# Optimization experiments

Measured on AMD Instinct MI355X. Metric: run time of the kernel, lower is better.

Reference implementation:

```python
import jax, jax.numpy as jnp
import numpy as np
import math

B_CH = 128   # bottleneck channels (conv1x1 in)
N_CH = 256   # encoder filters (conv1x1 out / linear in)
L = 16       # filter length (linear out); hop = L//2
BATCH = 8
K = 32000    # number of frames
T_ORIGIN = (L // 2) * (K - 1) + L  # 256008


def setup_inputs() -> dict:
    key = jax.random.key(0)
    k1, k2, k3, k4 = jax.random.split(key, 4)
    return {
        "mixture_w": jax.random.normal(k1, (BATCH, N_CH, K), jnp.float32),
        "est_mask": jax.random.normal(k2, (BATCH, B_CH, K), jnp.float32),
        "W_mask": jax.random.normal(k3, (N_CH, B_CH), jnp.float32) * (1.0 / np.sqrt(B_CH)),
        "W_basis": jax.random.normal(k4, (L, N_CH), jnp.float32) * (1.0 / np.sqrt(N_CH)),
        "T_origin": T_ORIGIN,
    }


def overlap_and_add(signal, frame_step):
    # signal: [..., frames, frame_length]
    frames, frame_length = signal.shape[-2], signal.shape[-1]
    sub_len = math.gcd(frame_length, frame_step)
    sub_step = frame_step // sub_len
    spf = frame_length // sub_len  # subframes per frame
    out_size = frame_step * (frames - 1) + frame_length
    out_sub = out_size // sub_len
    sub_sig = signal.reshape(signal.shape[:-2] + (frames * spf, sub_len))
    # scatter index for each subframe (same as torch unfold + index_add_)
    idx = (jnp.arange(frames)[:, None] * sub_step + jnp.arange(spf)[None, :]).reshape(-1)
    res = jnp.zeros(signal.shape[:-2] + (out_sub, sub_len), signal.dtype)
    res = res.at[..., idx, :].add(sub_sig)
    return res.reshape(signal.shape[:-2] + (out_size,))


def reference(mixture_w, est_mask, W_mask, W_basis, T_origin):
    # conv1x1 (bias-free) == channel matmul: [B_CH -> N_CH]
    m = jnp.einsum('nb,gbk->gnk', W_mask, est_mask)   # [batch, N, K]
    x = mixture_w * jax.nn.relu(m)                    # masked encoder output
    # transpose + Linear(N -> L, no bias): [batch, K, L]
    x = jnp.einsum('gnk,ln->gkl', x, W_basis)
    est_source = overlap_and_add(x, L // 2)           # [batch, T_conv]
    pad = T_origin - est_source.shape[-1]
    return jnp.pad(est_source, ((0, 0), (0, pad)))
```

## Files before the change

### kernel.cpp

```cpp
#include <hip/hip_runtime.h>
#include <stdint.h>

#define BATCH 8
#define NCH 256
#define BCH 128
#define KFR 32000
#define TOUT 256008
#define KT 32
#define NTPB 8
#define CHUNK (KT * NTPB)
#define NCHUNK (KFR / CHUNK)

typedef __attribute__((ext_vector_type(8))) short bf16x8;
typedef __attribute__((ext_vector_type(4))) float f32x4;

__device__ __forceinline__ unsigned short f32_to_bf16(float f) {
    unsigned int u = __builtin_bit_cast(unsigned int, f);
    u += 0x7FFFu + ((u >> 16) & 1u);
    return (unsigned short)(u >> 16);
}
__device__ __forceinline__ unsigned int pack2(float a, float b) {
    return (unsigned int)f32_to_bf16(a) | ((unsigned int)f32_to_bf16(b) << 16);
}
__device__ __forceinline__ f32x4 mload(const float* p) {
    f32x4 v;
    v[0] = p[0];
    v[1] = p[(size_t)KFR];
    v[2] = p[(size_t)2 * KFR];
    v[3] = p[(size_t)3 * KFR];
    return v;
}

__global__ void convert_weights(const float* __restrict__ Wm,
                                const float* __restrict__ Wb,
                                unsigned short* __restrict__ wbf) {
    int i = blockIdx.x * 256 + threadIdx.x;
    if (i < NCH * BCH) wbf[i] = f32_to_bf16(Wm[i]);
    if (i < 16 * NCH)  wbf[NCH * BCH + i] = f32_to_bf16(Wb[i]);
}

#define ESTT_W 68
#define XT_W 132
#define ESTT_WORDS (KT * ESTT_W)
#define XT_WORDS (KT * XT_W)
#define LOC_FLOATS (8 * CHUNK + 8)

#define G1(NT, FT, MM) { \
    const unsigned short* wr = wbf + (64 * wv + 16 * (NT) + l15) * BCH + 8 * lq; \
    bf16x8 w0 = *reinterpret_cast<const bf16x8*>(wr); \
    bf16x8 w1 = *reinterpret_cast<const bf16x8*>(wr + 32); \
    bf16x8 w2 = *reinterpret_cast<const bf16x8*>(wr + 64); \
    bf16x8 w3 = *reinterpret_cast<const bf16x8*>(wr + 96); \
    int f = 16 * (FT) + l15; \
    int msk = (2 * (FT) + (l15 >> 3)) & 3; \
    const unsigned short* br = estT + f * (2 * ESTT_W); \
    f32x4 a = {0.f, 0.f, 0.f, 0.f}; \
    a = __builtin_amdgcn_mfma_f32_16x16x32_bf16(w0, *reinterpret_cast<const bf16x8*>(br + 8 * ((0  + lq) ^ msk)), a, 0, 0, 0); \
    a = __builtin_amdgcn_mfma_f32_16x16x32_bf16(w1, *reinterpret_cast<const bf16x8*>(br + 8 * ((4  + lq) ^ msk)), a, 0, 0, 0); \
    a = __builtin_amdgcn_mfma_f32_16x16x32_bf16(w2, *reinterpret_cast<const bf16x8*>(br + 8 * ((8  + lq) ^ msk)), a, 0, 0, 0); \
    a = __builtin_amdgcn_mfma_f32_16x16x32_bf16(w3, *reinterpret_cast<const bf16x8*>(br + 8 * ((12 + lq) ^ msk)), a, 0, 0, 0); \
    float x0 = (a[0] > 0.f) ? (MM)[0] * a[0] : 0.f; \
    float x1 = (a[1] > 0.f) ? (MM)[1] * a[1] : 0.f; \
    float x2 = (a[2] > 0.f) ? (MM)[2] * a[2] : 0.f; \
    float x3 = (a[3] > 0.f) ? (MM)[3] * a[3] : 0.f; \
    int v = 8 * wv + 2 * (NT) + (lq >> 1); \
    uint2 uu; uu.x = pack2(x0, x1); uu.y = pack2(x2, x3); \
    *reinterpret_cast<uint2*>(xtd + f * XT_W + ((v ^ msk) << 2) + 2 * (lq & 1)) = uu; \
}

__global__ __launch_bounds__(256, 4)
void fused_decoder(const float* __restrict__ mix,
                   const float* __restrict__ est,
                   const unsigned short* __restrict__ wbf,
                   float* __restrict__ out) {
    __shared__ __align__(16) unsigned int smem[ESTT_WORDS + XT_WORDS + LOC_FLOATS];
    unsigned int* estd = smem;
    unsigned int* xtd  = smem + ESTT_WORDS;
    unsigned short* estT = reinterpret_cast<unsigned short*>(estd);
    unsigned short* xt   = reinterpret_cast<unsigned short*>(xtd);
    float* locout = reinterpret_cast<float*>(smem + ESTT_WORDS + XT_WORDS);

    const int tid = threadIdx.x;
    const int lane = tid & 63;
    const int wv = tid >> 6;
    const int l15 = lane & 15;
    const int lq = lane >> 4;
    const int f4 = tid & 7;
    const int rbase = tid >> 3;

    const int bid = blockIdx.x;
    const int g = bid / NCHUNK;
    const int c = bid % NCHUNK;

    const float* eg0 = est + ((size_t)g * BCH) * KFR + c * CHUNK;
    const float* mg0 = mix + ((size_t)g * NCH) * KFR + c * CHUNK;

    for (int s = tid; s < LOC_FLOATS / 4; s += 256) {
        f32x4 z = {0.f, 0.f, 0.f, 0.f};
        *reinterpret_cast<f32x4*>(locout + 4 * s) = z;
    }

    f32x4 er00, er01, er10, er11;
    {
        int bp0 = rbase, bp1 = 32 + rbase;
        er00 = *reinterpret_cast<const f32x4*>(eg0 + (size_t)(2 * bp0) * KFR + 4 * f4);
        er01 = *reinterpret_cast<const f32x4*>(eg0 + (size_t)(2 * bp0 + 1) * KFR + 4 * f4);
        er10 = *reinterpret_cast<const f32x4*>(eg0 + (size_t)(2 * bp1) * KFR + 4 * f4);
        er11 = *reinterpret_cast<const f32x4*>(eg0 + (size_t)(2 * bp1 + 1) * KFR + 4 * f4);
    }

    for (int t = 0; t < NTPB; ++t) {
        const float* mg = mg0 + t * KT;

        {
            int msk = (f4 >> 1) & 3;
            int base0 = (((rbase >> 2) ^ msk) << 2) + (rbase & 3);
            int base1 = ((((32 + rbase) >> 2) ^ msk) << 2) + ((32 + rbase) & 3);
#pragma unroll
            for (int i = 0; i < 4; ++i) {
                estd[(4 * f4 + i) * ESTT_W + base0] = pack2(er00[i], er01[i]);
                estd[(4 * f4 + i) * ESTT_W + base1] = pack2(er10[i], er11[i]);
            }
        }
        __syncthreads();

        const float* pm = mg + (size_t)(64 * wv + 4 * lq) * KFR + l15;
        f32x4 ma0 = mload(pm);
        f32x4 ma1 = mload(pm + (size_t)16 * KFR);
        f32x4 ma2 = mload(pm + (size_t)32 * KFR);
        f32x4 ma3 = mload(pm + (size_t)48 * KFR);
        G1(0, 0, ma0)
        G1(1, 0, ma1)
        f32x4 mb0 = mload(pm + 16);
        f32x4 mb1 = mload(pm + (size_t)16 * KFR + 16);
        f32x4 mb2 = mload(pm + (size_t)32 * KFR + 16);
        f32x4 mb3 = mload(pm + (size_t)48 * KFR + 16);
        G1(2, 0, ma2)
        G1(3, 0, ma3)
        G1(0, 1, mb0)
        G1(1, 1, mb1)
        G1(2, 1, mb2)
        G1(3, 1, mb3)
        __syncthreads();

        {
            const float* egn = eg0 + (t + 1 < NTPB ? (t + 1) * KT : t * KT);
            int bp0 = rbase, bp1 = 32 + rbase;
            er00 = *reinterpret_cast<const f32x4*>(egn + (size_t)(2 * bp0) * KFR + 4 * f4);
            er01 = *reinterpret_cast<const f32x4*>(egn + (size_t)(2 * bp0 + 1) * KFR + 4 * f4);
            er10 = *reinterpret_cast<const f32x4*>(egn + (size_t)(2 * bp1) * KFR + 4 * f4);
            er11 = *reinterpret_cast<const f32x4*>(egn + (size_t)(2 * bp1 + 1) * KFR + 4 * f4);
        }
        f32x4 acc2 = {0.f, 0.f, 0.f, 0.f};
        if (wv < 2) {
            int f = 16 * wv + l15;
            int msk = (2 * wv + (l15 >> 3)) & 3;
#pragma unroll
            for (int ks = 0; ks < 8; ++ks) {
                bf16x8 a = *reinterpret_cast<const bf16x8*>(
                    wbf + NCH * BCH + l15 * NCH + 32 * ks + 8 * lq);
                bf16x8 b = *reinterpret_cast<const bf16x8*>(
                    xt + f * (2 * XT_W) + 8 * ((4 * ks + lq) ^ msk));
                acc2 = __builtin_amdgcn_mfma_f32_16x16x32_bf16(a, b, acc2, 0, 0, 0);
            }
        }
        if (wv < 2 && lq < 2) {
            int f = 16 * wv + l15;
            int base = 256 * t + 8 * f + 4 * lq;
#pragma unroll
            for (int r = 0; r < 4; ++r) locout[base + r] += acc2[r];
        }
        __syncthreads();
        if (wv < 2 && lq >= 2) {
            int f = 16 * wv + l15;
            int base = 256 * t + 8 * f + 4 * lq;
#pragma unroll
            for (int r = 0; r < 4; ++r) locout[base + r] += acc2[r];
        }
    }
    __syncthreads();

    {
        float* og = out + (size_t)g * TOUT + (size_t)(8 * CHUNK) * c;
        for (int s = tid; s < LOC_FLOATS / 4; s += 256) {
            f32x4 v = *reinterpret_cast<const f32x4*>(locout + 4 * s);
            if (s >= 2 && s < (LOC_FLOATS / 4 - 2)) {
                *reinterpret_cast<f32x4*>(og + 4 * s) = v;
            } else {
#pragma unroll
                for (int r = 0; r < 4; ++r) atomicAdd(og + 4 * s + r, v[r]);
            }
        }
    }
}

extern "C" void kernel_launch(void* const* d_in, const int* in_sizes, int n_in,
                              void* d_out, int out_size, void* d_ws, size_t ws_size,
                              hipStream_t stream) {
    const float* mix = (const float*)d_in[0];
    const float* est = (const float*)d_in[1];
    const float* Wm  = (const float*)d_in[2];
    const float* Wb  = (const float*)d_in[3];
    unsigned short* wbf = (unsigned short*)d_ws;

    hipMemsetAsync(d_out, 0, (size_t)out_size * sizeof(float), stream);
    convert_weights<<<128, 256, 0, stream>>>(Wm, Wb, wbf);
    fused_decoder<<<BATCH * NCHUNK, 256, 0, stream>>>(mix, est, wbf, (float*)d_out);
}
```

Before: 140.5 us.

## Shrink per-block tile, drop LDS padding with XOR swizzle, shuffle-combine overlap-add

Result: slower. 304.4 us (+116.6%).

```diff
diff --git a/kernel.cpp b/kernel.cpp
--- a/kernel.cpp
+++ b/kernel.cpp
@@ -7,9 +7,12 @@
 #define KFR 32000
 #define TOUT 256008
 #define KT 32
-#define NTPB 8
+#define NTPB 5
 #define CHUNK (KT * NTPB)
 #define NCHUNK (KFR / CHUNK)
+#define ESTW 64
+#define XTW 128
+#define LOC_FLOATS (8 * CHUNK + 8)
 
 typedef __attribute__((ext_vector_type(8))) short bf16x8;
 typedef __attribute__((ext_vector_type(4))) float f32x4;
@@ -30,6 +33,9 @@
     v[3] = p[(size_t)3 * KFR];
     return v;
 }
+__device__ __forceinline__ int swz(int row, int w) {
+    return (((w >> 2) ^ (((row >> 2) & 3) << 1)) << 2) | (w & 3);
+}
 
 __global__ void convert_weights(const float* __restrict__ Wm,
                                 const float* __restrict__ Wb,
@@ -38,12 +44,6 @@
     if (i < NCH * BCH) wbf[i] = f32_to_bf16(Wm[i]);
     if (i < 16 * NCH)  wbf[NCH * BCH + i] = f32_to_bf16(Wb[i]);
 }
-
-#define ESTT_W 68
-#define XT_W 132
-#define ESTT_WORDS (KT * ESTT_W)
-#define XT_WORDS (KT * XT_W)
-#define LOC_FLOATS (8 * CHUNK + 8)
 
 #define G1(NT, FT, MM) { \
     const unsigned short* wr = wbf + (64 * wv + 16 * (NT) + l15) * BCH + 8 * lq; \
@@ -52,33 +52,31 @@
     bf16x8 w2 = *reinterpret_cast<const bf16x8*>(wr + 64); \
     bf16x8 w3 = *reinterpret_cast<const bf16x8*>(wr + 96); \
     int f = 16 * (FT) + l15; \
-    int msk = (2 * (FT) + (l15 >> 3)) & 3; \
-    const unsigned short* br = estT + f * (2 * ESTT_W); \
+    int sg = ((f >> 2) & 3) << 1; \
+    const unsigned int* br = estd + f * ESTW; \
     f32x4 a = {0.f, 0.f, 0.f, 0.f}; \
-    a = __builtin_amdgcn_mfma_f32_16x16x32_bf16(w0, *reinterpret_cast<const bf16x8*>(br + 8 * ((0  + lq) ^ msk)), a, 0, 0, 0); \
-    a = __builtin_amdgcn_mfma_f32_16x16x32_bf16(w1, *reinterpret_cast<const bf16x8*>(br + 8 * ((4  + lq) ^ msk)), a, 0, 0, 0); \
-    a = __builtin_amdgcn_mfma_f32_16x16x32_bf16(w2, *reinterpret_cast<const bf16x8*>(br + 8 * ((8  + lq) ^ msk)), a, 0, 0, 0); \
-    a = __builtin_amdgcn_mfma_f32_16x16x32_bf16(w3, *reinterpret_cast<const bf16x8*>(br + 8 * ((12 + lq) ^ msk)), a, 0, 0, 0); \
+    a = __builtin_amdgcn_mfma_f32_16x16x32_bf16(w0, *reinterpret_cast<const bf16x8*>(br + (((0  + lq) ^ sg) << 2)), a, 0, 0, 0); \
+    a = __builtin_amdgcn_mfma_f32_16x16x32_bf16(w1, *reinterpret_cast<const bf16x8*>(br + (((4  + lq) ^ sg) << 2)), a, 0, 0, 0); \
+    a = __builtin_amdgcn_mfma_f32_16x16x32_bf16(w2, *reinterpret_cast<const bf16x8*>(br + (((8  + lq) ^ sg) << 2)), a, 0, 0, 0); \
+    a = __builtin_amdgcn_mfma_f32_16x16x32_bf16(w3, *reinterpret_cast<const bf16x8*>(br + (((12 + lq) ^ sg) << 2)), a, 0, 0, 0); \
     float x0 = (a[0] > 0.f) ? (MM)[0] * a[0] : 0.f; \
     float x1 = (a[1] > 0.f) ? (MM)[1] * a[1] : 0.f; \
     float x2 = (a[2] > 0.f) ? (MM)[2] * a[2] : 0.f; \
     float x3 = (a[3] > 0.f) ? (MM)[3] * a[3] : 0.f; \
-    int v = 8 * wv + 2 * (NT) + (lq >> 1); \
+    int ue = 8 * wv + 2 * (NT) + (lq >> 1); \
     uint2 uu; uu.x = pack2(x0, x1); uu.y = pack2(x2, x3); \
-    *reinterpret_cast<uint2*>(xtd + f * XT_W + ((v ^ msk) << 2) + 2 * (lq & 1)) = uu; \
-}
-
-__global__ __launch_bounds__(256, 4)
+    *reinterpret_cast<uint2*>(xtd + f * XTW + (((ue ^ sg) << 2) | (2 * (lq & 1)))) = uu; \
+}
+
+__global__ __launch_bounds__(256, 5)
 void fused_decoder(const float* __restrict__ mix,
                    const float* __restrict__ est,
                    const unsigned short* __restrict__ wbf,
                    float* __restrict__ out) {
-    __shared__ __align__(16) unsigned int smem[ESTT_WORDS + XT_WORDS + LOC_FLOATS];
+    __shared__ __align__(16) unsigned int smem[32 * ESTW + 32 * XTW + LOC_FLOATS];
     unsigned int* estd = smem;
-    unsigned int* xtd  = smem + ESTT_WORDS;
-    unsigned short* estT = reinterpret_cast<unsigned short*>(estd);
-    unsigned short* xt   = reinterpret_cast<unsigned short*>(xtd);
-    float* locout = reinterpret_cast<float*>(smem + ESTT_WORDS + XT_WORDS);
+    unsigned int* xtd  = smem + 32 * ESTW;
+    float* locout = reinterpret_cast<float*>(smem + 32 * ESTW + 32 * XTW);
 
     const int tid = threadIdx.x;
     const int lane = tid & 63;
@@ -86,7 +84,7 @@
     const int l15 = lane & 15;
     const int lq = lane >> 4;
     const int f4 = tid & 7;
-    const int rbase = tid >> 3;
+    const int c0 = tid >> 3;
 
     const int bid = blockIdx.x;
     const int g = bid / NCHUNK;
@@ -102,25 +100,20 @@
 
     f32x4 er00, er01, er10, er11;
     {
-        int bp0 = rbase, bp1 = 32 + rbase;
-        er00 = *reinterpret_cast<const f32x4*>(eg0 + (size_t)(2 * bp0) * KFR + 4 * f4);
-        er01 = *reinterpret_cast<const f32x4*>(eg0 + (size_t)(2 * bp0 + 1) * KFR + 4 * f4);
-        er10 = *reinterpret_cast<const f32x4*>(eg0 + (size_t)(2 * bp1) * KFR + 4 * f4);
-        er11 = *reinterpret_cast<const f32x4*>(eg0 + (size_t)(2 * bp1 + 1) * KFR + 4 * f4);
+        er00 = *reinterpret_cast<const f32x4*>(eg0 + (size_t)(2 * c0) * KFR + 4 * f4);
+        er01 = *reinterpret_cast<const f32x4*>(eg0 + (size_t)(2 * c0 + 1) * KFR + 4 * f4);
+        er10 = *reinterpret_cast<const f32x4*>(eg0 + (size_t)(2 * c0 + 64) * KFR + 4 * f4);
+        er11 = *reinterpret_cast<const f32x4*>(eg0 + (size_t)(2 * c0 + 65) * KFR + 4 * f4);
     }
 
     for (int t = 0; t < NTPB; ++t) {
         const float* mg = mg0 + t * KT;
 
-        {
-            int msk = (f4 >> 1) & 3;
-            int base0 = (((rbase >> 2) ^ msk) << 2) + (rbase & 3);
-            int base1 = ((((32 + rbase) >> 2) ^ msk) << 2) + ((32 + rbase) & 3);
 #pragma unroll
-            for (int i = 0; i < 4; ++i) {
-                estd[(4 * f4 + i) * ESTT_W + base0] = pack2(er00[i], er01[i]);
-                estd[(4 * f4 + i) * ESTT_W + base1] = pack2(er10[i], er11[i]);
-            }
+        for (int i = 0; i < 4; ++i) {
+            int row = 4 * f4 + i;
+            estd[row * ESTW + swz(row, c0)]      = pack2(er00[i], er01[i]);
+            estd[row * ESTW + swz(row, c0 + 32)] = pack2(er10[i], er11[i]);
         }
         __syncthreads();
 
@@ -133,10 +126,10 @@
         G1(1, 0, ma1)
         f32x4 mb0 = mload(pm + 16);
         f32x4 mb1 = mload(pm + (size_t)16 * KFR + 16);
+        G1(2, 0, ma2)
+        G1(3, 0, ma3)
         f32x4 mb2 = mload(pm + (size_t)32 * KFR + 16);
         f32x4 mb3 = mload(pm + (size_t)48 * KFR + 16);
-        G1(2, 0, ma2)
-        G1(3, 0, ma3)
         G1(0, 1, mb0)
         G1(1, 1, mb1)
         G1(2, 1, mb2)
@@ -145,37 +138,46 @@
 
         {
             const float* egn = eg0 + (t + 1 < NTPB ? (t + 1) * KT : t * KT);
-            int bp0 = rbase, bp1 = 32 + rbase;
-            er00 = *reinterpret_cast<const f32x4*>(egn + (size_t)(2 * bp0) * KFR + 4 * f4);
-            er01 = *reinterpret_cast<const f32x4*>(egn + (size_t)(2 * bp0 + 1) * KFR + 4 * f4);
-            er10 = *reinterpret_cast<const f32x4*>(egn + (size_t)(2 * bp1) * KFR + 4 * f4);
-            er11 = *reinterpret_cast<const f32x4*>(egn + (size_t)(2 * bp1 + 1) * KFR + 4 * f4);
-        }
-        f32x4 acc2 = {0.f, 0.f, 0.f, 0.f};
+            er00 = *reinterpret_cast<const f32x4*>(egn + (size_t)(2 * c0) * KFR + 4 * f4);
+            er01 = *reinterpret_cast<const f32x4*>(egn + (size_t)(2 * c0 + 1) * KFR + 4 * f4);
+            er10 = *reinterpret_cast<const f32x4*>(egn + (size_t)(2 * c0 + 64) * KFR + 4 * f4);
+            er11 = *reinterpret_cast<const f32x4*>(egn + (size_t)(2 * c0 + 65) * KFR + 4 * f4);
+        }
         if (wv < 2) {
             int f = 16 * wv + l15;
-            int msk = (2 * wv + (l15 >> 3)) & 3;
+            int sg = ((f >> 2) & 3) << 1;
+            const unsigned int* br = xtd + f * XTW;
+            const unsigned short* wb2 = wbf + NCH * BCH + l15 * NCH + 8 * lq;
+            f32x4 acc2 = {0.f, 0.f, 0.f, 0.f};
 #pragma unroll
             for (int ks = 0; ks < 8; ++ks) {
-                bf16x8 a = *reinterpret_cast<const bf16x8*>(
-                    wbf + NCH * BCH + l15 * NCH + 32 * ks + 8 * lq);
-                bf16x8 b = *reinterpret_cast<const bf16x8*>(
-                    xt + f * (2 * XT_W) + 8 * ((4 * ks + lq) ^ msk));
+                bf16x8 a = *reinterpret_cast<const bf16x8*>(wb2 + 32 * ks);
+                bf16x8 b = *reinterpret_cast<const bf16x8*>(br + (((4 * ks + lq) ^ sg) << 2));
                 acc2 = __builtin_amdgcn_mfma_f32_16x16x32_bf16(a, b, acc2, 0, 0, 0);
             }
-        }
-        if (wv < 2 && lq < 2) {
-            int f = 16 * wv + l15;
-            int base = 256 * t + 8 * f + 4 * lq;
-#pragma unroll
-            for (int r = 0; r < 4; ++r) locout[base + r] += acc2[r];
-        }
-        __syncthreads();
-        if (wv < 2 && lq >= 2) {
-            int f = 16 * wv + l15;
-            int base = 256 * t + 8 * f + 4 * lq;
-#pragma unroll
-            for (int r = 0; r < 4; ++r) locout[base + r] += acc2[r];
+            int src = (lane + 31) & 63;
+            float p0 = __shfl(acc2[0], src, 64);
+            float p1 = __shfl(acc2[1], src, 64);
+            float p2 = __shfl(acc2[2], src, 64);
+            float p3 = __shfl(acc2[3], src, 64);
+            if (lq < 2) {
+                int toff = 256 * t + 8 * f + 4 * lq;
+                if (l15 == 0) {
+                    atomicAdd(locout + toff + 0, acc2[0]);
+                    atomicAdd(locout + toff + 1, acc2[1]);
+                    atomicAdd(locout + toff + 2, acc2[2]);
+                    atomicAdd(locout + toff + 3, acc2[3]);
+                } else {
+                    f32x4 s = {acc2[0] + p0, acc2[1] + p1, acc2[2] + p2, acc2[3] + p3};
+                    *reinterpret_cast<f32x4*>(locout + toff) = s;
+                }
+            } else if (l15 == 15) {
+                int toff = 256 * t + 8 * (16 * wv + 16) + 4 * (lq - 2);
+                atomicAdd(locout + toff + 0, acc2[0]);
+                atomicAdd(locout + toff + 1, acc2[1]);
+                atomicAdd(locout + toff + 2, acc2[2]);
+                atomicAdd(locout + toff + 3, acc2[3]);
+            }
         }
     }
     __syncthreads();
```
